# Optimization experiments

Hardware: AMD Instinct MI355X
Metric: run time of the kernel (lower is better)

Reference implementation:

```python
import jax, jax.numpy as jnp
import numpy as np

N_NODES = 100_000
N_EDGES = 800_000
D_EDGE = 64
D_NODE = 64
D_GLOBAL = 64
D_IN = D_EDGE + 2 * D_NODE + D_GLOBAL  # 256
D_HID = 128
D_OUT = 64


def setup_inputs() -> dict:
    key = jax.random.key(0)
    ks = jax.random.split(key, 8)
    edge_feats = jax.random.normal(ks[0], (N_EDGES, D_EDGE), dtype=jnp.float32)
    node_feats = jax.random.normal(ks[1], (N_NODES, D_NODE), dtype=jnp.float32)
    global_attr = jax.random.normal(ks[2], (D_GLOBAL,), dtype=jnp.float32)
    senders = jax.random.randint(ks[3], (N_EDGES,), 0, N_NODES, dtype=jnp.int32)
    receivers = jax.random.randint(ks[4], (N_EDGES,), 0, N_NODES, dtype=jnp.int32)
    W1 = jax.random.normal(ks[5], (D_IN, D_HID), dtype=jnp.float32) * (1.0 / np.sqrt(D_IN))
    b1 = jnp.zeros((D_HID,), dtype=jnp.float32)
    W2 = jax.random.normal(ks[6], (D_HID, D_OUT), dtype=jnp.float32) * (1.0 / np.sqrt(D_HID))
    b2 = jnp.zeros((D_OUT,), dtype=jnp.float32)
    return {
        "edge_feats": edge_feats,
        "node_feats": node_feats,
        "global_attr": global_attr,
        "senders": senders,
        "receivers": receivers,
        "W1": W1, "b1": b1, "W2": W2, "b2": b2,
    }


def reference(edge_feats, node_feats, global_attr, senders, receivers, W1, b1, W2, b2):
    # Per-edge concat of [edge.data, receiver.data, sender.data, global.data]
    # (torch.cat order in the original), stacked over all edges.
    E = edge_feats.shape[0]
    recv = node_feats[receivers]          # [E, D_NODE] gather
    send = node_feats[senders]            # [E, D_NODE] gather
    g = jnp.broadcast_to(global_attr[None, :], (E, global_attr.shape[0]))
    x = jnp.concatenate([edge_feats, recv, send, g], axis=-1)  # [E, 256]
    # Updater MLP on the stacked edge batch.
    h = jax.nn.relu(x @ W1 + b1)          # [E, 128]
    out = h @ W2 + b2                     # [E, 64]
    return out
```

## Files before the change

### kernel.cpp

```cpp
#include <hip/hip_runtime.h>
#include <hip/hip_bf16.h>


typedef __bf16 bf16x8 __attribute__((ext_vector_type(8)));
typedef float f32x4 __attribute__((ext_vector_type(4)));

#define GRID_MAIN 2048
#define WS_NODEBF_OFF 66560

__global__ void prep_kernel(const float* __restrict__ W1, const float* __restrict__ b1,
                            const float* __restrict__ W2, const float* __restrict__ gattr,
                            __bf16* __restrict__ W1F, __bf16* __restrict__ W2F,
                            float* __restrict__ g1) {
    int tid = blockIdx.x * blockDim.x + threadIdx.x;
    if (tid < 128 * 192) {
        int n = tid / 192, k = tid % 192;
        int w = n >> 5, nt2 = (n >> 4) & 1, c = n & 15;
        int f = k >> 5, g = (k >> 3) & 3, j = k & 7;
        W1F[((((w * 2 + nt2) * 6 + f) * 64) + c + 16 * g) * 8 + j] = (__bf16)W1[k * 128 + n];
    } else if (tid < 128 * 192 + 64 * 128) {
        int t = tid - 128 * 192;
        int n = t / 128, k = t % 128;
        int w = n >> 4, c = n & 15;
        int ks = k >> 5, g = (k >> 3) & 3, j = k & 7;
        W2F[(((w * 4 + ks) * 64) + c + 16 * g) * 8 + j] = (__bf16)W2[k * 64 + n];
    } else if (tid < 128 * 192 + 64 * 128 + 128) {
        int n = tid - (128 * 192 + 64 * 128);
        float acc = b1[n];
        for (int j = 0; j < 64; ++j) acc += gattr[j] * W1[(192 + j) * 128 + n];
        g1[n] = acc;
    }
}

__global__ __launch_bounds__(256) void node_conv_kernel(const float* __restrict__ nf,
                                                        __bf16* __restrict__ nb, int n8) {
    int t = blockIdx.x * blockDim.x + threadIdx.x;
    if (t < n8) {
        f32x4 a = *(const f32x4*)(nf + (long)t * 8);
        f32x4 b = *(const f32x4*)(nf + (long)t * 8 + 4);
        bf16x8 o;
#pragma unroll
        for (int j = 0; j < 4; ++j) { o[j] = (__bf16)a[j]; o[4 + j] = (__bf16)b[j]; }
        *(bf16x8*)(nb + (long)t * 8) = o;
    }
}

__device__ __forceinline__ f32x4 mk4(float v) {
    f32x4 r; r[0] = v; r[1] = v; r[2] = v; r[3] = v; return r;
}

__device__ __forceinline__ bf16x8 cvt8(f32x4 lo, f32x4 hi) {
    bf16x8 t;
#pragma unroll
    for (int j = 0; j < 4; ++j) { t[j] = (__bf16)lo[j]; t[4 + j] = (__bf16)hi[j]; }
    return t;
}

__global__ __launch_bounds__(256) void edge_mlp_kernel(
    const float* __restrict__ edge_feats, const __bf16* __restrict__ node_bf,
    const int* __restrict__ senders, const int* __restrict__ receivers,
    const __bf16* __restrict__ W1F, const __bf16* __restrict__ W2F,
    const float* __restrict__ g1, const float* __restrict__ b2,
    float* __restrict__ out, int E, int numTiles)
{
    __shared__ __bf16 A_lds[4 * 6 * 64 * 8];
    __shared__ __bf16 h_lds[64][136];

    const int lane = threadIdx.x & 63;
    const int w    = threadIdx.x >> 6;
    const int c    = lane & 15;
    const int g    = lane >> 4;
    const int G    = gridDim.x;

    bf16x8 wb1[2][6];
#pragma unroll
    for (int nt2 = 0; nt2 < 2; ++nt2)
#pragma unroll
        for (int f = 0; f < 6; ++f)
            wb1[nt2][f] = *(const bf16x8*)(W1F + (((w * 2 + nt2) * 6 + f) * 64 + lane) * 8);
    bf16x8 wb2[4];
#pragma unroll
    for (int ks = 0; ks < 4; ++ks)
        wb2[ks] = *(const bf16x8*)(W2F + ((w * 4 + ks) * 64 + lane) * 8);
    const float g1v0 = g1[w * 32 + c];
    const float g1v1 = g1[w * 32 + 16 + c];
    const float b2v  = b2[w * 16 + c];

    int curR = 0, curS = 0;
    {
        long rc = (long)blockIdx.x * 64 + w * 16 + c;
        if (rc > (long)E - 1) rc = (long)E - 1;
        curR = receivers[rc]; curS = senders[rc];
    }

    for (int t = blockIdx.x; t < numTiles; t += G) {
        const __bf16* pr = node_bf + ((long)curR << 6) + g * 8;
        const __bf16* ps = node_bf + ((long)curS << 6) + g * 8;
        bf16x8 nr0 = *(const bf16x8*)(pr);
        bf16x8 nr1 = *(const bf16x8*)(pr + 32);
        bf16x8 ns0 = *(const bf16x8*)(ps);
        bf16x8 ns1 = *(const bf16x8*)(ps + 32);

        long rowc = (long)t * 64 + w * 16 + c;
        if (rowc > (long)E - 1) rowc = (long)E - 1;
        const float* pe = edge_feats + (rowc << 6) + g * 8;
        f32x4 e0a = *(const f32x4*)(pe);
        f32x4 e0b = *(const f32x4*)(pe + 4);
        f32x4 e1a = *(const f32x4*)(pe + 32);
        f32x4 e1b = *(const f32x4*)(pe + 36);

        int tn = t + G;
        if (tn < numTiles) {
            long rc2 = (long)tn * 64 + w * 16 + c;
            if (rc2 > (long)E - 1) rc2 = (long)E - 1;
            curR = receivers[rc2]; curS = senders[rc2];
        }

        __bf16* ab = A_lds + (w * 6) * 64 * 8 + lane * 8;
        *(bf16x8*)(ab)           = cvt8(e0a, e0b);
        *(bf16x8*)(ab + 512)     = cvt8(e1a, e1b);
        *(bf16x8*)(ab + 1024)    = nr0;
        *(bf16x8*)(ab + 1536)    = nr1;
        *(bf16x8*)(ab + 2048)    = ns0;
        *(bf16x8*)(ab + 2560)    = ns1;
        __syncthreads();

        f32x4 acc0[4], acc1[4];
#pragma unroll
        for (int mt = 0; mt < 4; ++mt) { acc0[mt] = mk4(g1v0); acc1[mt] = mk4(g1v1); }
#pragma unroll
        for (int mt = 0; mt < 4; ++mt)
#pragma unroll
            for (int f = 0; f < 6; ++f) {
                bf16x8 a = *(const bf16x8*)(A_lds + ((mt * 6 + f) * 64 + lane) * 8);
                acc0[mt] = __builtin_amdgcn_mfma_f32_16x16x32_bf16(a, wb1[0][f], acc0[mt], 0, 0, 0);
                acc1[mt] = __builtin_amdgcn_mfma_f32_16x16x32_bf16(a, wb1[1][f], acc1[mt], 0, 0, 0);
            }

#pragma unroll
        for (int mt = 0; mt < 4; ++mt)
#pragma unroll
            for (int r = 0; r < 4; ++r) {
                float v0 = acc0[mt][r]; v0 = v0 > 0.f ? v0 : 0.f;
                float v1 = acc1[mt][r]; v1 = v1 > 0.f ? v1 : 0.f;
                h_lds[mt * 16 + g * 4 + r][w * 32 + c]      = (__bf16)v0;
                h_lds[mt * 16 + g * 4 + r][w * 32 + 16 + c] = (__bf16)v1;
            }
        __syncthreads();

        f32x4 acc2[4];
#pragma unroll
        for (int mt = 0; mt < 4; ++mt) acc2[mt] = mk4(b2v);
#pragma unroll
        for (int mt = 0; mt < 4; ++mt)
#pragma unroll
            for (int ks = 0; ks < 4; ++ks) {
                bf16x8 ah = *(const bf16x8*)&h_lds[mt * 16 + c][ks * 32 + g * 8];
                acc2[mt] = __builtin_amdgcn_mfma_f32_16x16x32_bf16(ah, wb2[ks], acc2[mt], 0, 0, 0);
            }

#pragma unroll
        for (int mt = 0; mt < 4; ++mt)
#pragma unroll
            for (int r = 0; r < 4; ++r) {
                long orow = (long)t * 64 + mt * 16 + g * 4 + r;
                if (orow < E) out[orow * 64 + w * 16 + c] = acc2[mt][r];
            }
        __syncthreads();
    }
}

__global__ __launch_bounds__(256) void edge_mlp_fallback(
    const float* __restrict__ edge_feats, const float* __restrict__ node_feats,
    const int* __restrict__ senders, const int* __restrict__ receivers,
    const __bf16* __restrict__ W1F, const __bf16* __restrict__ W2F,
    const float* __restrict__ g1, const float* __restrict__ b2,
    float* __restrict__ out, int E, int numTiles)
{
    __shared__ __bf16 A_lds[4 * 6 * 64 * 8];
    __shared__ __bf16 h_lds[64][136];
    const int lane = threadIdx.x & 63;
    const int w = threadIdx.x >> 6;
    const int c = lane & 15;
    const int g = lane >> 4;
    const int G = gridDim.x;

    bf16x8 wb1[2][6];
#pragma unroll
    for (int nt2 = 0; nt2 < 2; ++nt2)
#pragma unroll
        for (int f = 0; f < 6; ++f)
            wb1[nt2][f] = *(const bf16x8*)(W1F + (((w * 2 + nt2) * 6 + f) * 64 + lane) * 8);
    bf16x8 wb2[4];
#pragma unroll
    for (int ks = 0; ks < 4; ++ks)
        wb2[ks] = *(const bf16x8*)(W2F + ((w * 4 + ks) * 64 + lane) * 8);
    const float g1v0 = g1[w * 32 + c];
    const float g1v1 = g1[w * 32 + 16 + c];
    const float b2v  = b2[w * 16 + c];

    for (int t = blockIdx.x; t < numTiles; t += G) {
        long rowc = (long)t * 64 + w * 16 + c;
        if (rowc > (long)E - 1) rowc = (long)E - 1;
        int iR = receivers[rowc], iS = senders[rowc];
        const float* pr = node_feats + ((long)iR << 6) + g * 8;
        const float* ps = node_feats + ((long)iS << 6) + g * 8;
        const float* pe = edge_feats + (rowc << 6) + g * 8;
        f32x4 e0a = *(const f32x4*)(pe),      e0b = *(const f32x4*)(pe + 4);
        f32x4 e1a = *(const f32x4*)(pe + 32), e1b = *(const f32x4*)(pe + 36);
        f32x4 r0a = *(const f32x4*)(pr),      r0b = *(const f32x4*)(pr + 4);
        f32x4 r1a = *(const f32x4*)(pr + 32), r1b = *(const f32x4*)(pr + 36);
        f32x4 s0a = *(const f32x4*)(ps),      s0b = *(const f32x4*)(ps + 4);
        f32x4 s1a = *(const f32x4*)(ps + 32), s1b = *(const f32x4*)(ps + 36);

        __bf16* ab = A_lds + (w * 6) * 64 * 8 + lane * 8;
        *(bf16x8*)(ab)        = cvt8(e0a, e0b);
        *(bf16x8*)(ab + 512)  = cvt8(e1a, e1b);
        *(bf16x8*)(ab + 1024) = cvt8(r0a, r0b);
        *(bf16x8*)(ab + 1536) = cvt8(r1a, r1b);
        *(bf16x8*)(ab + 2048) = cvt8(s0a, s0b);
        *(bf16x8*)(ab + 2560) = cvt8(s1a, s1b);
        __syncthreads();

        f32x4 acc0[4], acc1[4];
#pragma unroll
        for (int mt = 0; mt < 4; ++mt) { acc0[mt] = mk4(g1v0); acc1[mt] = mk4(g1v1); }
#pragma unroll
        for (int mt = 0; mt < 4; ++mt)
#pragma unroll
            for (int f = 0; f < 6; ++f) {
                bf16x8 a = *(const bf16x8*)(A_lds + ((mt * 6 + f) * 64 + lane) * 8);
                acc0[mt] = __builtin_amdgcn_mfma_f32_16x16x32_bf16(a, wb1[0][f], acc0[mt], 0, 0, 0);
                acc1[mt] = __builtin_amdgcn_mfma_f32_16x16x32_bf16(a, wb1[1][f], acc1[mt], 0, 0, 0);
            }
#pragma unroll
        for (int mt = 0; mt < 4; ++mt)
#pragma unroll
            for (int r = 0; r < 4; ++r) {
                float v0 = acc0[mt][r]; v0 = v0 > 0.f ? v0 : 0.f;
                float v1 = acc1[mt][r]; v1 = v1 > 0.f ? v1 : 0.f;
                h_lds[mt * 16 + g * 4 + r][w * 32 + c]      = (__bf16)v0;
                h_lds[mt * 16 + g * 4 + r][w * 32 + 16 + c] = (__bf16)v1;
            }
        __syncthreads();

        f32x4 acc2[4];
#pragma unroll
        for (int mt = 0; mt < 4; ++mt) acc2[mt] = mk4(b2v);
#pragma unroll
        for (int mt = 0; mt < 4; ++mt)
#pragma unroll
            for (int ks = 0; ks < 4; ++ks) {
                bf16x8 ah = *(const bf16x8*)&h_lds[mt * 16 + c][ks * 32 + g * 8];
                acc2[mt] = __builtin_amdgcn_mfma_f32_16x16x32_bf16(ah, wb2[ks], acc2[mt], 0, 0, 0);
            }
#pragma unroll
        for (int mt = 0; mt < 4; ++mt)
#pragma unroll
            for (int r = 0; r < 4; ++r) {
                long orow = (long)t * 64 + mt * 16 + g * 4 + r;
                if (orow < E) out[orow * 64 + w * 16 + c] = acc2[mt][r];
            }
        __syncthreads();
    }
}

extern "C" void kernel_launch(void* const* d_in, const int* in_sizes, int n_in,
                              void* d_out, int out_size, void* d_ws, size_t ws_size,
                              hipStream_t stream) {
    const float* edge_feats = (const float*)d_in[0];
    const float* node_feats = (const float*)d_in[1];
    const float* gattr      = (const float*)d_in[2];
    const int*   senders    = (const int*)d_in[3];
    const int*   receivers  = (const int*)d_in[4];
    const float* W1         = (const float*)d_in[5];
    const float* b1         = (const float*)d_in[6];
    const float* W2         = (const float*)d_in[7];
    const float* b2         = (const float*)d_in[8];
    float* out = (float*)d_out;

    const int E = in_sizes[3];
    const int N = in_sizes[1] / 64;

    char* ws = (char*)d_ws;
    __bf16* W1F = (__bf16*)ws;
    __bf16* W2F = (__bf16*)(ws + 49152);
    float*  g1  = (float*)(ws + 49152 + 16384);
    __bf16* nodeBF = (__bf16*)(ws + WS_NODEBF_OFF);

    const size_t ws_needed = (size_t)WS_NODEBF_OFF + (size_t)N * 64 * 2;
    const bool useNB = ws_size >= ws_needed;

    int prep_total = 128 * 192 + 64 * 128 + 128;
    prep_kernel<<<(prep_total + 255) / 256, 256, 0, stream>>>(W1, b1, W2, gattr, W1F, W2F, g1);

    const int numTiles = (E + 63) / 64;
    int grid = numTiles < GRID_MAIN ? numTiles : GRID_MAIN;
    if (useNB) {
        int n8 = N * 8;
        node_conv_kernel<<<(n8 + 255) / 256, 256, 0, stream>>>(node_feats, nodeBF, n8);
        edge_mlp_kernel<<<grid, 256, 0, stream>>>(edge_feats, nodeBF, senders, receivers,
                                                  W1F, W2F, g1, b2, out, E, numTiles);
    } else {
        edge_mlp_fallback<<<grid, 256, 0, stream>>>(edge_feats, node_feats, senders, receivers,
                                                    W1F, W2F, g1, b2, out, E, numTiles);
    }
}
```

Baseline: 125.4 us.

## Prefetch next tile's gathers into registers and repack hidden layer into MFMA fragments

The main edge kernel now issues the global loads for the next tile's edge features and gathered node rows before the current tile's MFMA work, so gather latency overlaps with compute. The hidden activations are written to LDS as packed bf16 pairs in a fragment-ordered layout, with W2's K dimension permuted to match, which should give contiguous conflict-free reads for the second GEMM. __syncthreads is replaced with explicit lgkmcnt waits plus s_barrier so outstanding global loads are not drained at each barrier. The cost is higher register pressure from holding the prefetched data, and correctness now depends on the W2 permutation matching the h layout.

```diff
diff --git a/kernel.cpp b/kernel.cpp
--- a/kernel.cpp
+++ b/kernel.cpp
@@ -3,6 +3,7 @@
 
 
 typedef __bf16 bf16x8 __attribute__((ext_vector_type(8)));
+typedef __bf16 bf16x2 __attribute__((ext_vector_type(2)));
 typedef float f32x4 __attribute__((ext_vector_type(4)));
 
 #define GRID_MAIN 2048
@@ -20,10 +21,11 @@
         W1F[((((w * 2 + nt2) * 6 + f) * 64) + c + 16 * g) * 8 + j] = (__bf16)W1[k * 128 + n];
     } else if (tid < 128 * 192 + 64 * 128) {
         int t = tid - 128 * 192;
-        int n = t / 128, k = t % 128;
+        int n = t / 128, p = t % 128;
         int w = n >> 4, c = n & 15;
-        int ks = k >> 5, g = (k >> 3) & 3, j = k & 7;
-        W2F[(((w * 4 + ks) * 64) + c + 16 * g) * 8 + j] = (__bf16)W2[k * 64 + n];
+        int ks = p >> 5, g = (p >> 3) & 3, j = p & 7;
+        int klog = (p >> 5) * 32 + (p & 1) * 16 + ((p >> 1) & 15);
+        W2F[(((w * 4 + ks) * 64) + c + 16 * g) * 8 + j] = (__bf16)W2[klog * 64 + n];
     } else if (tid < 128 * 192 + 64 * 128 + 128) {
         int n = tid - (128 * 192 + 64 * 128);
         float acc = b1[n];
@@ -64,7 +66,7 @@
     float* __restrict__ out, int E, int numTiles)
 {
     __shared__ __bf16 A_lds[4 * 6 * 64 * 8];
-    __shared__ __bf16 h_lds[64][136];
+    __shared__ __bf16 h_frag[4 * 4 * 64 * 8];
 
     const int lane = threadIdx.x & 63;
     const int w    = threadIdx.x >> 6;
@@ -86,44 +88,61 @@
     const float g1v1 = g1[w * 32 + 16 + c];
     const float b2v  = b2[w * 16 + c];
 
-    int curR = 0, curS = 0;
+    bf16x8 snr0, snr1, sns0, sns1;
+    f32x4 se0, se1, se2, se3;
+    int iR, iS;
     {
         long rc = (long)blockIdx.x * 64 + w * 16 + c;
         if (rc > (long)E - 1) rc = (long)E - 1;
-        curR = receivers[rc]; curS = senders[rc];
+        iR = receivers[rc]; iS = senders[rc];
+        const __bf16* pr = node_bf + ((long)iR << 6) + g * 8;
+        const __bf16* ps = node_bf + ((long)iS << 6) + g * 8;
+        snr0 = *(const bf16x8*)(pr);
+        snr1 = *(const bf16x8*)(pr + 32);
+        sns0 = *(const bf16x8*)(ps);
+        sns1 = *(const bf16x8*)(ps + 32);
+        const float* pe = edge_feats + (rc << 6) + g * 8;
+        se0 = *(const f32x4*)(pe);      se1 = *(const f32x4*)(pe + 4);
+        se2 = *(const f32x4*)(pe + 32); se3 = *(const f32x4*)(pe + 36);
+        if (blockIdx.x + G < numTiles) {
+            long rc2 = (long)(blockIdx.x + G) * 64 + w * 16 + c;
+            if (rc2 > (long)E - 1) rc2 = (long)E - 1;
+            iR = receivers[rc2]; iS = senders[rc2];
+        }
     }
 
     for (int t = blockIdx.x; t < numTiles; t += G) {
-        const __bf16* pr = node_bf + ((long)curR << 6) + g * 8;
-        const __bf16* ps = node_bf + ((long)curS << 6) + g * 8;
-        bf16x8 nr0 = *(const bf16x8*)(pr);
-        bf16x8 nr1 = *(const bf16x8*)(pr + 32);
-        bf16x8 ns0 = *(const bf16x8*)(ps);
-        bf16x8 ns1 = *(const bf16x8*)(ps + 32);
-
-        long rowc = (long)t * 64 + w * 16 + c;
-        if (rowc > (long)E - 1) rowc = (long)E - 1;
-        const float* pe = edge_feats + (rowc << 6) + g * 8;
-        f32x4 e0a = *(const f32x4*)(pe);
-        f32x4 e0b = *(const f32x4*)(pe + 4);
-        f32x4 e1a = *(const f32x4*)(pe + 32);
-        f32x4 e1b = *(const f32x4*)(pe + 36);
-
-        int tn = t + G;
+        __bf16* ab = A_lds + w * 6 * 512 + lane * 8;
+        *(bf16x8*)(ab)        = cvt8(se0, se1);
+        *(bf16x8*)(ab + 512)  = cvt8(se2, se3);
+        *(bf16x8*)(ab + 1024) = snr0;
+        *(bf16x8*)(ab + 1536) = snr1;
+        *(bf16x8*)(ab + 2048) = sns0;
+        *(bf16x8*)(ab + 2560) = sns1;
+
+        const int tn = t + G;
         if (tn < numTiles) {
-            long rc2 = (long)tn * 64 + w * 16 + c;
-            if (rc2 > (long)E - 1) rc2 = (long)E - 1;
-            curR = receivers[rc2]; curS = senders[rc2];
+            const __bf16* pr = node_bf + ((long)iR << 6) + g * 8;
+            const __bf16* ps = node_bf + ((long)iS << 6) + g * 8;
+            snr0 = *(const bf16x8*)(pr);
+            snr1 = *(const bf16x8*)(pr + 32);
+            sns0 = *(const bf16x8*)(ps);
+            sns1 = *(const bf16x8*)(ps + 32);
+            long rce = (long)tn * 64 + w * 16 + c;
+            if (rce > (long)E - 1) rce = (long)E - 1;
+            const float* pe = edge_feats + (rce << 6) + g * 8;
+            se0 = *(const f32x4*)(pe);      se1 = *(const f32x4*)(pe + 4);
+            se2 = *(const f32x4*)(pe + 32); se3 = *(const f32x4*)(pe + 36);
+            if (tn + G < numTiles) {
+                long rc2 = (long)(tn + G) * 64 + w * 16 + c;
+                if (rc2 > (long)E - 1) rc2 = (long)E - 1;
+                iR = receivers[rc2]; iS = senders[rc2];
+            }
         }
-
-        __bf16* ab = A_lds + (w * 6) * 64 * 8 + lane * 8;
-        *(bf16x8*)(ab)           = cvt8(e0a, e0b);
-        *(bf16x8*)(ab + 512)     = cvt8(e1a, e1b);
-        *(bf16x8*)(ab + 1024)    = nr0;
-        *(bf16x8*)(ab + 1536)    = nr1;
-        *(bf16x8*)(ab + 2048)    = ns0;
-        *(bf16x8*)(ab + 2560)    = ns1;
-        __syncthreads();
+        __builtin_amdgcn_sched_barrier(0);
+
+        asm volatile("s_waitcnt lgkmcnt(0)" ::: "memory");
+        __builtin_amdgcn_s_barrier();
 
         f32x4 acc0[4], acc1[4];
 #pragma unroll
@@ -143,10 +162,13 @@
             for (int r = 0; r < 4; ++r) {
                 float v0 = acc0[mt][r]; v0 = v0 > 0.f ? v0 : 0.f;
                 float v1 = acc1[mt][r]; v1 = v1 > 0.f ? v1 : 0.f;
-                h_lds[mt * 16 + g * 4 + r][w * 32 + c]      = (__bf16)v0;
-                h_lds[mt * 16 + g * 4 + r][w * 32 + 16 + c] = (__bf16)v1;
-            }
-        __syncthreads();
+                bf16x2 pk; pk[0] = (__bf16)v0; pk[1] = (__bf16)v1;
+                *(bf16x2*)&h_frag[(((mt * 4 + w) * 64 + (g * 4 + r) * 4 + (c >> 2)) << 3)
+                                  + ((c & 3) << 1)] = pk;
+            }
+
+        asm volatile("s_waitcnt lgkmcnt(0)" ::: "memory");
+        __builtin_amdgcn_s_barrier();
 
         f32x4 acc2[4];
 #pragma unroll
@@ -155,7 +177,7 @@
         for (int mt = 0; mt < 4; ++mt)
 #pragma unroll
             for (int ks = 0; ks < 4; ++ks) {
-                bf16x8 ah = *(const bf16x8*)&h_lds[mt * 16 + c][ks * 32 + g * 8];
+                bf16x8 ah = *(const bf16x8*)&h_frag[((mt * 4 + ks) * 64 + c * 4 + g) * 8];
                 acc2[mt] = __builtin_amdgcn_mfma_f32_16x16x32_bf16(ah, wb2[ks], acc2[mt], 0, 0, 0);
             }
 
@@ -166,7 +188,9 @@
                 long orow = (long)t * 64 + mt * 16 + g * 4 + r;
                 if (orow < E) out[orow * 64 + w * 16 + c] = acc2[mt][r];
             }
-        __syncthreads();
+
+        asm volatile("s_waitcnt lgkmcnt(0)" ::: "memory");
+        __builtin_amdgcn_s_barrier();
     }
 }
 
@@ -178,7 +202,7 @@
     float* __restrict__ out, int E, int numTiles)
 {
     __shared__ __bf16 A_lds[4 * 6 * 64 * 8];
-    __shared__ __bf16 h_lds[64][136];
+    __shared__ __bf16 h_frag[4 * 4 * 64 * 8];
     const int lane = threadIdx.x & 63;
     const int w = threadIdx.x >> 6;
     const int c = lane & 15;
@@ -213,7 +237,7 @@
         f32x4 s0a = *(const f32x4*)(ps),      s0b = *(const f32x4*)(ps + 4);
         f32x4 s1a = *(const f32x4*)(ps + 32), s1b = *(const f32x4*)(ps + 36);
 
-        __bf16* ab = A_lds + (w * 6) * 64 * 8 + lane * 8;
+        __bf16* ab = A_lds + w * 6 * 512 + lane * 8;
         *(bf16x8*)(ab)        = cvt8(e0a, e0b);
         *(bf16x8*)(ab + 512)  = cvt8(e1a, e1b);
         *(bf16x8*)(ab + 1024) = cvt8(r0a, r0b);
@@ -239,8 +263,9 @@
             for (int r = 0; r < 4; ++r) {
                 float v0 = acc0[mt][r]; v0 = v0 > 0.f ? v0 : 0.f;
                 float v1 = acc1[mt][r]; v1 = v1 > 0.f ? v1 : 0.f;
-                h_lds[mt * 16 + g * 4 + r][w * 32 + c]      = (__bf16)v0;
-                h_lds[mt * 16 + g * 4 + r][w * 32 + 16 + c] = (__bf16)v1;
+                bf16x2 pk; pk[0] = (__bf16)v0; pk[1] = (__bf16)v1;
+                *(bf16x2*)&h_frag[(((mt * 4 + w) * 64 + (g * 4 + r) * 4 + (c >> 2)) << 3)
+                                  + ((c & 3) << 1)] = pk;
             }
         __syncthreads();
 
@@ -251,7 +276,7 @@
         for (int mt = 0; mt < 4; ++mt)
 #pragma unroll
             for (int ks = 0; ks < 4; ++ks) {
-                bf16x8 ah = *(const bf16x8*)&h_lds[mt * 16 + c][ks * 32 + g * 8];
+                bf16x8 ah = *(const bf16x8*)&h_frag[((mt * 4 + ks) * 64 + c * 4 + g) * 8];
                 acc2[mt] = __builtin_amdgcn_mfma_f32_16x16x32_bf16(ah, wb2[ks], acc2[mt], 0, 0, 0);
             }
 #pragma unroll
```

Measured after the change: 124.0 us. About the same (-1.1%).
